# Kernel tuning notes

Hardware: AMD Instinct MI355X
Metric: run time of the kernel (lower is better)

## Reference

```python
import jax, jax.numpy as jnp
import numpy as np
import math

B, S, D = 2, 2048, 768
H, KS, VS = 12, 64, 64
MAX_DIST, NUM_BASES, MIN_HALF_LIFE = 1000, 16, 3.0


def _exponential_basis_features():
    # positions -max_dist..max_dist, exponential basis as in RelativePositionalBias
    positions = np.arange(-MAX_DIST, MAX_DIST + 1)
    abs_pos = np.abs(positions).astype(np.float32)
    max_range = math.log2(MAX_DIST)
    half_lives = np.power(2.0, np.linspace(MIN_HALF_LIFE, max_range, NUM_BASES)).reshape(1, -1)
    feats = np.exp(-math.log(2.0) * abs_pos[:, None] / half_lives)  # [2*max_dist+1, num_bases]
    return jnp.asarray(feats, dtype=jnp.float32)


def setup_inputs() -> dict:
    key = jax.random.key(0)
    ks = jax.random.split(key, 6)
    x = jax.random.normal(ks[0], (B, S, D), dtype=jnp.float32)
    # torch nn.Linear weight convention: [out_features, in_features], applied as x @ W.T
    Wq = jax.random.normal(ks[1], (H * KS, D), dtype=jnp.float32) * 0.02
    Wk = jax.random.normal(ks[2], (H * KS, D), dtype=jnp.float32) * 0.02
    Wv = jax.random.normal(ks[3], (H * VS, D), dtype=jnp.float32) * 0.02
    # original zero-inits w_o; use small random for a non-degenerate correctness baseline
    Wo = jax.random.normal(ks[4], (D, H * VS), dtype=jnp.float32) * 0.02
    basis_weights = jax.random.normal(ks[5], (H, NUM_BASES), dtype=jnp.float32)
    basis_features = _exponential_basis_features()  # buffer (non-learned)
    return {"x": x, "Wq": Wq, "Wk": Wk, "Wv": Wv, "Wo": Wo,
            "basis_weights": basis_weights, "basis_features": basis_features}


def _relative_bias(basis_features, basis_weights, q_len, k_len):
    rel = jnp.arange(k_len)[None, :] - jnp.arange(q_len)[:, None]
    rel = jnp.clip(rel, -MAX_DIST, MAX_DIST) + MAX_DIST  # [q, k] indices
    basis = basis_features[rel]                          # [q, k, nb]
    return jnp.einsum('qkb,hb->hqk', basis, basis_weights)


def reference(x, Wq, Wk, Wv, Wo, basis_weights, basis_features):
    b, s, _ = x.shape
    q = (x @ Wq.T).reshape(b, s, H, KS)
    k = (x @ Wk.T).reshape(b, s, H, KS)
    v = (x @ Wv.T).reshape(b, s, H, VS)
    scale = math.sqrt(KS)
    scores = jnp.einsum('bqhc,bkhc->bhqk', q, k) / scale
    scores = scores + _relative_bias(basis_features, basis_weights, s, s)[None]
    attn = jax.nn.softmax(scores, axis=-1)  # dropout is identity in eval
    out = jnp.einsum('bhqk,bkhv->bqhv', attn, v).reshape(b, s, H * VS)
    out = out @ Wo.T
    return out, attn
```

## Files before the change

### kernel.cpp

```cpp
#include <hip/hip_runtime.h>

typedef _Float16 f16;
typedef __attribute__((ext_vector_type(8))) _Float16 f16x8;
typedef __attribute__((ext_vector_type(4))) float f32x4;
typedef __attribute__((ext_vector_type(16))) float f32x16;

#define B_ 2
#define S_ 2048
#define DMODEL 768
#define H_ 12
#define HS 64
#define NB_ 16
#define QKV_LD 2304

#define ZERO16 {0.f,0.f,0.f,0.f,0.f,0.f,0.f,0.f,0.f,0.f,0.f,0.f,0.f,0.f,0.f,0.f}

__global__ __launch_bounds__(256) void cast_f16_kernel(const float* __restrict__ in,
                                                       f16* __restrict__ out,
                                                       int n4, float scale) {
    int i = blockIdx.x * 256 + threadIdx.x;
    if (i >= n4) return;
    float4 v = reinterpret_cast<const float4*>(in)[i];
    union { f16 h[4]; unsigned long long u; } o;
    o.h[0] = (f16)(v.x * scale);
    o.h[1] = (f16)(v.y * scale);
    o.h[2] = (f16)(v.z * scale);
    o.h[3] = (f16)(v.w * scale);
    reinterpret_cast<unsigned long long*>(out)[i] = o.u;
}

__global__ __launch_bounds__(256) void bias_table_kernel(const float* __restrict__ bw,
                                                         const float* __restrict__ bf,
                                                         float* __restrict__ tab) {
    int idx = blockIdx.x * 256 + threadIdx.x;
    if (idx >= H_ * 4095) return;
    int h = idx / 4095, d = idx % 4095;
    int rel = d - 2047;
    rel = min(1000, max(-1000, rel));
    int r = rel + 1000;
    float s = 0.f;
#pragma unroll
    for (int t = 0; t < NB_; ++t) s += bf[r * NB_ + t] * bw[h * NB_ + t];
    tab[h * 4095 + d] = s * 1.44269504088896f;
}

template <typename OutT>
__global__ __launch_bounds__(256) void gemm_nt(const f16* __restrict__ A,
                                               const f16* __restrict__ Bm,
                                               OutT* __restrict__ C,
                                               int M, int N, int K, float alpha) {
    __shared__ __align__(16) f16 As[128][32];
    __shared__ __align__(16) f16 Bs[128][32];
    const int tiles_n = N >> 7;
    int tm = blockIdx.x / tiles_n, tn = blockIdx.x % tiles_n;
    int m0 = tm << 7, n0 = tn << 7;
    int t = threadIdx.x;
    int w = t >> 6, l = t & 63;
    int wr = w >> 1, wc = w & 1;
    int fr = l & 15, fc = (l >> 4) << 3;
    f32x4 acc[4][4] = {};

    for (int k0 = 0; k0 < K; k0 += 32) {
#pragma unroll
        for (int uu = 0; uu < 2; ++uu) {
            int u = t + uu * 256;
            int row = u >> 2, c = (u & 3) << 3;
            *reinterpret_cast<f16x8*>(&As[row][c]) =
                *reinterpret_cast<const f16x8*>(&A[(size_t)(m0 + row) * K + k0 + c]);
            *reinterpret_cast<f16x8*>(&Bs[row][c]) =
                *reinterpret_cast<const f16x8*>(&Bm[(size_t)(n0 + row) * K + k0 + c]);
        }
        __syncthreads();
        f16x8 af[4], bfv[4];
#pragma unroll
        for (int m = 0; m < 4; ++m)
            af[m] = *reinterpret_cast<const f16x8*>(&As[wr * 64 + m * 16 + fr][fc]);
#pragma unroll
        for (int n = 0; n < 4; ++n)
            bfv[n] = *reinterpret_cast<const f16x8*>(&Bs[wc * 64 + n * 16 + fr][fc]);
#pragma unroll
        for (int m = 0; m < 4; ++m)
#pragma unroll
            for (int n = 0; n < 4; ++n)
                acc[m][n] = __builtin_amdgcn_mfma_f32_16x16x32_f16(af[m], bfv[n], acc[m][n], 0, 0, 0);
        __syncthreads();
    }
    int cc = l & 15, cr = (l >> 4) << 2;
#pragma unroll
    for (int m = 0; m < 4; ++m)
#pragma unroll
        for (int n = 0; n < 4; ++n)
#pragma unroll
            for (int j = 0; j < 4; ++j) {
                int rg = m0 + wr * 64 + m * 16 + cr + j;
                int cg = n0 + wc * 64 + n * 16 + cc;
                C[(size_t)rg * N + cg] = (OutT)(acc[m][n][j] * alpha);
            }
}

__global__ __launch_bounds__(256, 3) void attn_kernel(const f16* __restrict__ qp,
                                                      const f16* __restrict__ kp,
                                                      const f16* __restrict__ vp,
                                                      const float* __restrict__ biasTab,
                                                      float* __restrict__ attn_out,
                                                      f16* __restrict__ ctx_out) {
    __shared__ __align__(16) f16 Ks[64][72];
    __shared__ __align__(16) f16 VsT[64][72];
    __shared__ __align__(16) f16 psh[64][72];
    __shared__ float bias_l[2112];
    __shared__ float red_m[64][2], red_l[64][2];
    __shared__ float m_s[64], li_s[64];

    int orig = blockIdx.x;
    int blk = (orig & 7) * 96 + (orig >> 3);
    int qt = blk & 31;
    int bh = blk >> 5;
    int h = bh % H_;
    int b = bh / H_;
    int q0 = qt << 6;

    int t = threadIdx.x;
    int w = t >> 6, l = t & 63;
    int wq = w >> 1, wk = w & 1;
    int col = l & 31;
    int hi = l >> 5;
    int hi4 = hi << 2, hi8 = hi << 3;

    const size_t rowbase = (size_t)b * S_ * QKV_LD + (size_t)h * HS;

    f16x8 qf[4];
    {
        const f16* qrow = qp + rowbase + (size_t)(q0 + wq * 32 + col) * QKV_LD + hi8;
#pragma unroll
        for (int ci = 0; ci < 4; ++ci) qf[ci] = *reinterpret_cast<const f16x8*>(qrow + ci * 16);
    }

    {
        const float* bt = biasTab + h * 4095 + (1984 - q0);
        for (int i = t; i < 2112; i += 256) bias_l[i] = bt[i];
    }

    float mreg[16], lreg[16];
#pragma unroll
    for (int r = 0; r < 16; ++r) { mreg[r] = -3.0e38f; lreg[r] = 0.f; }

    for (int kb0 = 0; kb0 < S_; kb0 += 64) {
        {
            int row = t >> 3, c = (t & 7) << 3;
            const f16* kb = kp + rowbase + (size_t)(kb0 + row) * QKV_LD + c;
            *reinterpret_cast<f16x8*>(&Ks[row][c]) = *reinterpret_cast<const f16x8*>(kb);
            *reinterpret_cast<f16x8*>(&Ks[row + 32][c]) =
                *reinterpret_cast<const f16x8*>(kb + (size_t)32 * QKV_LD);
        }
        __syncthreads();
        f32x16 s = ZERO16;
#pragma unroll
        for (int ci = 0; ci < 4; ++ci) {
            f16x8 kf = *reinterpret_cast<const f16x8*>(&Ks[wk * 32 + col][ci * 16 + hi8]);
            s = __builtin_amdgcn_mfma_f32_32x32x16_f16(qf[ci], kf, s, 0, 0, 0);
        }
        int kcol = kb0 + wk * 32 + col;
        const float* bl = bias_l + (kcol - (wq * 32 + hi4) + 63);
#pragma unroll
        for (int r = 0; r < 16; ++r) {
            const int cr = (r & 3) + 8 * (r >> 2);
            float sv = s[r] + bl[-cr];
            float d = sv - mreg[r];
            float e = __builtin_amdgcn_exp2f(-fabsf(d));
            bool up = d > 0.f;
            lreg[r] = up ? (lreg[r] * e + 1.f) : (lreg[r] + e);
            mreg[r] = up ? sv : mreg[r];
        }
        __syncthreads();
    }

#pragma unroll
    for (int off = 1; off < 32; off <<= 1) {
#pragma unroll
        for (int r = 0; r < 16; ++r) {
            float mo = __shfl_xor(mreg[r], off);
            float lo = __shfl_xor(lreg[r], off);
            float mn = fmaxf(mreg[r], mo);
            lreg[r] = lreg[r] * __builtin_amdgcn_exp2f(mreg[r] - mn)
                    + lo * __builtin_amdgcn_exp2f(mo - mn);
            mreg[r] = mn;
        }
    }
    if (col == 0) {
#pragma unroll
        for (int r = 0; r < 16; ++r) {
            int row = wq * 32 + (r & 3) + 8 * (r >> 2) + hi4;
            red_m[row][wk] = mreg[r];
            red_l[row][wk] = lreg[r];
        }
    }
    __syncthreads();
    if (t < 64) {
        float m0 = red_m[t][0], m1 = red_m[t][1];
        float mf = fmaxf(m0, m1);
        float lf = red_l[t][0] * __builtin_amdgcn_exp2f(m0 - mf)
                 + red_l[t][1] * __builtin_amdgcn_exp2f(m1 - mf);
        m_s[t] = mf;
        li_s[t] = 1.0f / lf;
    }
    __syncthreads();
#pragma unroll
    for (int r = 0; r < 16; ++r) {
        int row = wq * 32 + (r & 3) + 8 * (r >> 2) + hi4;
        mreg[r] = m_s[row];
        lreg[r] = li_s[row];
    }

    f32x16 oacc = ZERO16;
    float* aout = attn_out + (((size_t)b * H_ + h) * S_ + q0) * S_;

    for (int kb0 = 0; kb0 < S_; kb0 += 64) {
        {
            int row = t >> 3, c = (t & 7) << 3;
            const f16* kb = kp + rowbase + (size_t)(kb0 + row) * QKV_LD + c;
            *reinterpret_cast<f16x8*>(&Ks[row][c]) = *reinterpret_cast<const f16x8*>(kb);
            *reinterpret_cast<f16x8*>(&Ks[row + 32][c]) =
                *reinterpret_cast<const f16x8*>(kb + (size_t)32 * QKV_LD);
            int cv = t >> 2, v0 = (t & 3) << 4;
            const f16* src = vp + rowbase + (size_t)(kb0 + cv) * QKV_LD + v0;
            __align__(16) f16 tmp[16];
            *reinterpret_cast<f16x8*>(tmp)     = *reinterpret_cast<const f16x8*>(src);
            *reinterpret_cast<f16x8*>(tmp + 8) = *reinterpret_cast<const f16x8*>(src + 8);
#pragma unroll
            for (int i2 = 0; i2 < 16; ++i2) VsT[v0 + i2][cv] = tmp[i2];
        }
        __syncthreads();
        f32x16 s = ZERO16;
#pragma unroll
        for (int ci = 0; ci < 4; ++ci) {
            f16x8 kf = *reinterpret_cast<const f16x8*>(&Ks[wk * 32 + col][ci * 16 + hi8]);
            s = __builtin_amdgcn_mfma_f32_32x32x16_f16(qf[ci], kf, s, 0, 0, 0);
        }
        int kcol = kb0 + wk * 32 + col;
        const float* bl = bias_l + (kcol - (wq * 32 + hi4) + 63);
#pragma unroll
        for (int r = 0; r < 16; ++r) {
            const int cr = (r & 3) + 8 * (r >> 2);
            int row = wq * 32 + cr + hi4;
            float sv = s[r] + bl[-cr];
            float p = __builtin_amdgcn_exp2f(sv - mreg[r]) * lreg[r];
            aout[(size_t)row * S_ + kcol] = p;
            psh[row][wk * 32 + col] = (f16)p;
        }
        __syncthreads();
#pragma unroll
        for (int ci = 0; ci < 4; ++ci) {
            f16x8 pa = *reinterpret_cast<const f16x8*>(&psh[wq * 32 + col][ci * 16 + hi8]);
            f16x8 vf = *reinterpret_cast<const f16x8*>(&VsT[wk * 32 + col][ci * 16 + hi8]);
            oacc = __builtin_amdgcn_mfma_f32_32x32x16_f16(pa, vf, oacc, 0, 0, 0);
        }
        __syncthreads();
    }

    {
        f16* cbase = ctx_out + ((size_t)b * S_ + q0) * DMODEL + h * HS + wk * 32 + col;
#pragma unroll
        for (int r = 0; r < 16; ++r) {
            int row = wq * 32 + (r & 3) + 8 * (r >> 2) + hi4;
            cbase[(size_t)row * DMODEL] = (f16)oacc[r];
        }
    }
}

extern "C" void kernel_launch(void* const* d_in, const int* in_sizes, int n_in,
                              void* d_out, int out_size, void* d_ws, size_t ws_size,
                              hipStream_t stream) {
    const float* x     = (const float*)d_in[0];
    const float* Wq    = (const float*)d_in[1];
    const float* Wk    = (const float*)d_in[2];
    const float* Wv    = (const float*)d_in[3];
    const float* Wo    = (const float*)d_in[4];
    const float* bw    = (const float*)d_in[5];
    const float* bfeat = (const float*)d_in[6];

    char* ws = (char*)d_ws;
    f16*   xb      = (f16*)(ws + 0);
    f16*   qkv     = (f16*)(ws + 6291456);
    f16*   ctx     = (f16*)(ws + 25165824);
    f16*   wqkv16  = (f16*)(ws + 31457280);
    f16*   wo16    = (f16*)(ws + 34996224);
    float* biasTab = (float*)(ws + 36175872);

    float* out0 = (float*)d_out;
    float* attn = out0 + (size_t)B_ * S_ * DMODEL;

    cast_f16_kernel<<<3072, 256, 0, stream>>>(x, xb, 786432, 1.0f);
    cast_f16_kernel<<<576, 256, 0, stream>>>(Wq, wqkv16 + 0,        147456, 0.18033688011112f);
    cast_f16_kernel<<<576, 256, 0, stream>>>(Wk, wqkv16 + 589824,   147456, 1.0f);
    cast_f16_kernel<<<576, 256, 0, stream>>>(Wv, wqkv16 + 1179648,  147456, 1.0f);
    cast_f16_kernel<<<576, 256, 0, stream>>>(Wo, wo16,              147456, 1.0f);
    bias_table_kernel<<<192, 256, 0, stream>>>(bw, bfeat, biasTab);

    gemm_nt<f16><<<32 * 18, 256, 0, stream>>>(xb, wqkv16, qkv, 4096, QKV_LD, 768, 1.0f);

    attn_kernel<<<B_ * H_ * (S_ / 64), 256, 0, stream>>>(
        qkv + 0, qkv + 768, qkv + 1536, biasTab, attn, ctx);

    gemm_nt<float><<<32 * 6, 256, 0, stream>>>(ctx, wo16, out0, 4096, DMODEL, 768, 1.0f);
}
```

Baseline: 211.1 us.

## Drop online max in softmax, merge weight casts, pad GEMM LDS, stream attn stores

```diff
diff --git a/kernel.cpp b/kernel.cpp
--- a/kernel.cpp
+++ b/kernel.cpp
@@ -29,6 +29,26 @@
     reinterpret_cast<unsigned long long*>(out)[i] = o.u;
 }
 
+__global__ __launch_bounds__(256) void wcast_kernel(const float* __restrict__ Wq,
+                                                    const float* __restrict__ Wk,
+                                                    const float* __restrict__ Wv,
+                                                    f16* __restrict__ dst) {
+    int i = blockIdx.x * 256 + threadIdx.x;
+    const float* src;
+    float scale = 1.0f;
+    int j = i;
+    if (i < 147456)      { src = Wq; scale = 0.18033688011112f; }
+    else if (i < 294912) { src = Wk; j = i - 147456; }
+    else                 { src = Wv; j = i - 294912; }
+    float4 v = reinterpret_cast<const float4*>(src)[j];
+    union { f16 h[4]; unsigned long long u; } o;
+    o.h[0] = (f16)(v.x * scale);
+    o.h[1] = (f16)(v.y * scale);
+    o.h[2] = (f16)(v.z * scale);
+    o.h[3] = (f16)(v.w * scale);
+    reinterpret_cast<unsigned long long*>(dst)[i] = o.u;
+}
+
 __global__ __launch_bounds__(256) void bias_table_kernel(const float* __restrict__ bw,
                                                          const float* __restrict__ bf,
                                                          float* __restrict__ tab) {
@@ -49,8 +69,8 @@
                                                const f16* __restrict__ Bm,
                                                OutT* __restrict__ C,
                                                int M, int N, int K, float alpha) {
-    __shared__ __align__(16) f16 As[128][32];
-    __shared__ __align__(16) f16 Bs[128][32];
+    __shared__ __align__(16) f16 As[128][40];
+    __shared__ __align__(16) f16 Bs[128][40];
     const int tiles_n = N >> 7;
     int tm = blockIdx.x / tiles_n, tn = blockIdx.x % tiles_n;
     int m0 = tm << 7, n0 = tn << 7;
@@ -98,18 +118,20 @@
             }
 }
 
-__global__ __launch_bounds__(256, 3) void attn_kernel(const f16* __restrict__ qp,
+__global__ __launch_bounds__(256, 4) void attn_kernel(const f16* __restrict__ qp,
                                                       const f16* __restrict__ kp,
                                                       const f16* __restrict__ vp,
                                                       const float* __restrict__ biasTab,
                                                       float* __restrict__ attn_out,
                                                       f16* __restrict__ ctx_out) {
-    __shared__ __align__(16) f16 Ks[64][72];
-    __shared__ __align__(16) f16 VsT[64][72];
+    __shared__ union {
+        f16 ks1[128][72];
+        struct { f16 ks[64][72]; f16 vst[64][72]; } p2;
+    } ar;
     __shared__ __align__(16) f16 psh[64][72];
     __shared__ float bias_l[2112];
-    __shared__ float red_m[64][2], red_l[64][2];
-    __shared__ float m_s[64], li_s[64];
+    __shared__ float red_l[64][2];
+    __shared__ float li_s[64];
 
     int orig = blockIdx.x;
     int blk = (orig & 7) * 96 + (orig >> 3);
@@ -137,89 +159,68 @@
 
     {
         const float* bt = biasTab + h * 4095 + (1984 - q0);
-        for (int i = t; i < 2112; i += 256) bias_l[i] = bt[i];
-    }
-
-    float mreg[16], lreg[16];
-#pragma unroll
-    for (int r = 0; r < 16; ++r) { mreg[r] = -3.0e38f; lreg[r] = 0.f; }
+        for (int i = t; i < 2111; i += 256) bias_l[i] = bt[i];
+    }
+
+    float lsum[16];
+#pragma unroll
+    for (int r = 0; r < 16; ++r) lsum[r] = 0.f;
+
+    for (int kb0 = 0; kb0 < S_; kb0 += 128) {
+#pragma unroll
+        for (int uu = 0; uu < 4; ++uu) {
+            int u = (uu << 8) + t;
+            int row = u >> 3, c = (u & 7) << 3;
+            *reinterpret_cast<f16x8*>(&ar.ks1[row][c]) =
+                *reinterpret_cast<const f16x8*>(kp + rowbase + (size_t)(kb0 + row) * QKV_LD + c);
+        }
+        __syncthreads();
+#pragma unroll
+        for (int half = 0; half < 2; ++half) {
+            f32x16 s = ZERO16;
+#pragma unroll
+            for (int ci = 0; ci < 4; ++ci) {
+                f16x8 kf = *reinterpret_cast<const f16x8*>(
+                    &ar.ks1[half * 64 + wk * 32 + col][ci * 16 + hi8]);
+                s = __builtin_amdgcn_mfma_f32_32x32x16_f16(qf[ci], kf, s, 0, 0, 0);
+            }
+            int kcol = kb0 + half * 64 + wk * 32 + col;
+            const float* bl = bias_l + (kcol + 63 - (wq * 32 + hi4));
+#pragma unroll
+            for (int r = 0; r < 16; ++r) {
+                const int cr = (r & 3) + 8 * (r >> 2);
+                lsum[r] += __builtin_amdgcn_exp2f(s[r] + bl[-cr]);
+            }
+        }
+        __syncthreads();
+    }
+
+#pragma unroll
+    for (int off = 1; off < 32; off <<= 1) {
+#pragma unroll
+        for (int r = 0; r < 16; ++r) lsum[r] += __shfl_xor(lsum[r], off);
+    }
+    if (col == 0) {
+#pragma unroll
+        for (int r = 0; r < 16; ++r)
+            red_l[wq * 32 + (r & 3) + 8 * (r >> 2) + hi4][wk] = lsum[r];
+    }
+    __syncthreads();
+    if (t < 64) li_s[t] = 1.0f / (red_l[t][0] + red_l[t][1]);
+    __syncthreads();
+    float lreg[16];
+#pragma unroll
+    for (int r = 0; r < 16; ++r) lreg[r] = li_s[wq * 32 + (r & 3) + 8 * (r >> 2) + hi4];
+
+    f32x16 oacc = ZERO16;
+    float* aout = attn_out + (((size_t)b * H_ + h) * S_ + q0) * S_;
 
     for (int kb0 = 0; kb0 < S_; kb0 += 64) {
         {
             int row = t >> 3, c = (t & 7) << 3;
             const f16* kb = kp + rowbase + (size_t)(kb0 + row) * QKV_LD + c;
-            *reinterpret_cast<f16x8*>(&Ks[row][c]) = *reinterpret_cast<const f16x8*>(kb);
-            *reinterpret_cast<f16x8*>(&Ks[row + 32][c]) =
-                *reinterpret_cast<const f16x8*>(kb + (size_t)32 * QKV_LD);
-        }
-        __syncthreads();
-        f32x16 s = ZERO16;
-#pragma unroll
-        for (int ci = 0; ci < 4; ++ci) {
-            f16x8 kf = *reinterpret_cast<const f16x8*>(&Ks[wk * 32 + col][ci * 16 + hi8]);
-            s = __builtin_amdgcn_mfma_f32_32x32x16_f16(qf[ci], kf, s, 0, 0, 0);
-        }
-        int kcol = kb0 + wk * 32 + col;
-        const float* bl = bias_l + (kcol - (wq * 32 + hi4) + 63);
-#pragma unroll
-        for (int r = 0; r < 16; ++r) {
-            const int cr = (r & 3) + 8 * (r >> 2);
-            float sv = s[r] + bl[-cr];
-            float d = sv - mreg[r];
-            float e = __builtin_amdgcn_exp2f(-fabsf(d));
-            bool up = d > 0.f;
-            lreg[r] = up ? (lreg[r] * e + 1.f) : (lreg[r] + e);
-            mreg[r] = up ? sv : mreg[r];
-        }
-        __syncthreads();
-    }
-
-#pragma unroll
-    for (int off = 1; off < 32; off <<= 1) {
-#pragma unroll
-        for (int r = 0; r < 16; ++r) {
-            float mo = __shfl_xor(mreg[r], off);
-            float lo = __shfl_xor(lreg[r], off);
-            float mn = fmaxf(mreg[r], mo);
-            lreg[r] = lreg[r] * __builtin_amdgcn_exp2f(mreg[r] - mn)
-                    + lo * __builtin_amdgcn_exp2f(mo - mn);
-            mreg[r] = mn;
-        }
-    }
-    if (col == 0) {
-#pragma unroll
-        for (int r = 0; r < 16; ++r) {
-            int row = wq * 32 + (r & 3) + 8 * (r >> 2) + hi4;
-            red_m[row][wk] = mreg[r];
-            red_l[row][wk] = lreg[r];
-        }
-    }
-    __syncthreads();
-    if (t < 64) {
-        float m0 = red_m[t][0], m1 = red_m[t][1];
-        float mf = fmaxf(m0, m1);
-        float lf = red_l[t][0] * __builtin_amdgcn_exp2f(m0 - mf)
-                 + red_l[t][1] * __builtin_amdgcn_exp2f(m1 - mf);
-        m_s[t] = mf;
-        li_s[t] = 1.0f / lf;
-    }
-    __syncthreads();
-#pragma unroll
-    for (int r = 0; r < 16; ++r) {
-        int row = wq * 32 + (r & 3) + 8 * (r >> 2) + hi4;
-        mreg[r] = m_s[row];
-        lreg[r] = li_s[row];
-    }
-
-    f32x16 oacc = ZERO16;
-    float* aout = attn_out + (((size_t)b * H_ + h) * S_ + q0) * S_;
-
-    for (int kb0 = 0; kb0 < S_; kb0 += 64) {
-        {
-            int row = t >> 3, c = (t & 7) << 3;
-            const f16* kb = kp + rowbase + (size_t)(kb0 + row) * QKV_LD + c;
-            *reinterpret_cast<f16x8*>(&Ks[row][c]) = *reinterpret_cast<const f16x8*>(kb);
-            *reinterpret_cast<f16x8*>(&Ks[row + 32][c]) =
+            *reinterpret_cast<f16x8*>(&ar.p2.ks[row][c]) = *reinterpret_cast<const f16x8*>(kb);
+            *reinterpret_cast<f16x8*>(&ar.p2.ks[row + 32][c]) =
                 *reinterpret_cast<const f16x8*>(kb + (size_t)32 * QKV_LD);
             int cv = t >> 2, v0 = (t & 3) << 4;
             const f16* src = vp + rowbase + (size_t)(kb0 + cv) * QKV_LD + v0;
@@ -227,31 +228,30 @@
             *reinterpret_cast<f16x8*>(tmp)     = *reinterpret_cast<const f16x8*>(src);
             *reinterpret_cast<f16x8*>(tmp + 8) = *reinterpret_cast<const f16x8*>(src + 8);
 #pragma unroll
-            for (int i2 = 0; i2 < 16; ++i2) VsT[v0 + i2][cv] = tmp[i2];
+            for (int i2 = 0; i2 < 16; ++i2) ar.p2.vst[v0 + i2][cv] = tmp[i2];
         }
         __syncthreads();
         f32x16 s = ZERO16;
 #pragma unroll
         for (int ci = 0; ci < 4; ++ci) {
-            f16x8 kf = *reinterpret_cast<const f16x8*>(&Ks[wk * 32 + col][ci * 16 + hi8]);
+            f16x8 kf = *reinterpret_cast<const f16x8*>(&ar.p2.ks[wk * 32 + col][ci * 16 + hi8]);
             s = __builtin_amdgcn_mfma_f32_32x32x16_f16(qf[ci], kf, s, 0, 0, 0);
         }
         int kcol = kb0 + wk * 32 + col;
-        const float* bl = bias_l + (kcol - (wq * 32 + hi4) + 63);
+        const float* bl = bias_l + (kcol + 63 - (wq * 32 + hi4));
 #pragma unroll
         for (int r = 0; r < 16; ++r) {
             const int cr = (r & 3) + 8 * (r >> 2);
             int row = wq * 32 + cr + hi4;
-            float sv = s[r] + bl[-cr];
-            float p = __builtin_amdgcn_exp2f(sv - mreg[r]) * lreg[r];
-            aout[(size_t)row * S_ + kcol] = p;
+            float p = __builtin_amdgcn_exp2f(s[r] + bl[-cr]) * lreg[r];
+            __builtin_nontemporal_store(p, &aout[(size_t)row * S_ + kcol]);
             psh[row][wk * 32 + col] = (f16)p;
         }
         __syncthreads();
 #pragma unroll
         for (int ci = 0; ci < 4; ++ci) {
             f16x8 pa = *reinterpret_cast<const f16x8*>(&psh[wq * 32 + col][ci * 16 + hi8]);
-            f16x8 vf = *reinterpret_cast<const f16x8*>(&VsT[wk * 32 + col][ci * 16 + hi8]);
+            f16x8 vf = *reinterpret_cast<const f16x8*>(&ar.p2.vst[wk * 32 + col][ci * 16 + hi8]);
             oacc = __builtin_amdgcn_mfma_f32_32x32x16_f16(pa, vf, oacc, 0, 0, 0);
         }
         __syncthreads();
@@ -290,10 +290,8 @@
     float* attn = out0 + (size_t)B_ * S_ * DMODEL;
 
     cast_f16_kernel<<<3072, 256, 0, stream>>>(x, xb, 786432, 1.0f);
-    cast_f16_kernel<<<576, 256, 0, stream>>>(Wq, wqkv16 + 0,        147456, 0.18033688011112f);
-    cast_f16_kernel<<<576, 256, 0, stream>>>(Wk, wqkv16 + 589824,   147456, 1.0f);
-    cast_f16_kernel<<<576, 256, 0, stream>>>(Wv, wqkv16 + 1179648,  147456, 1.0f);
-    cast_f16_kernel<<<576, 256, 0, stream>>>(Wo, wo16,              147456, 1.0f);
+    wcast_kernel<<<1728, 256, 0, stream>>>(Wq, Wk, Wv, wqkv16);
+    cast_f16_kernel<<<576, 256, 0, stream>>>(Wo, wo16, 147456, 1.0f);
     bias_table_kernel<<<192, 256, 0, stream>>>(bw, bfeat, biasTab);
 
     gemm_nt<f16><<<32 * 18, 256, 0, stream>>>(xb, wqkv16, qkv, 4096, QKV_LD, 768, 1.0f);
```

Measured after the change: 198.0 us. 1.07x faster.
